# Kernel optimization log

Measured on AMD Instinct MI355X. Metric: run time of the kernel, lower is better.

## Reference

```python
import jax, jax.numpy as jnp
import numpy as np

B, S, N = 1, 128, 256
C_IN, C_H, C_OUT = 256, 32, 128
EPS = 1e-5


def setup_inputs() -> dict:
    key = jax.random.key(0)
    k_m, k_wa, k_wb, k_wo = jax.random.split(key, 4)
    m = jax.random.normal(k_m, (B, S, N, C_IN), dtype=jnp.float32)
    mask = jnp.ones((B, S, N), dtype=jnp.float32)
    gamma = jnp.ones((C_IN,), dtype=jnp.float32)
    beta = jnp.zeros((C_IN,), dtype=jnp.float32)
    # nn.Linear weights are (out, in)
    Wa = jax.random.normal(k_wa, (C_H, C_IN), dtype=jnp.float32) / np.sqrt(C_IN).astype(np.float32)
    Wb = jax.random.normal(k_wb, (C_H, C_IN), dtype=jnp.float32) / np.sqrt(C_IN).astype(np.float32)
    # proj_o is final_init (zeros) in the source; use small random weights so the
    # baseline output is non-trivial for correctness checking.
    Wo = jax.random.normal(k_wo, (C_OUT, C_H * C_H), dtype=jnp.float32) / np.sqrt(C_H * C_H).astype(np.float32)
    bo = jnp.zeros((C_OUT,), dtype=jnp.float32)
    return {"m": m, "mask": mask, "gamma": gamma, "beta": beta,
            "Wa": Wa, "Wb": Wb, "Wo": Wo, "bo": bo}


def reference(m, mask, gamma, beta, Wa, Wb, Wo, bo):
    # LayerNorm over c_in
    mu = jnp.mean(m, axis=-1, keepdims=True)
    var = jnp.mean((m - mu) ** 2, axis=-1, keepdims=True)
    mn = (m - mu) * jax.lax.rsqrt(var + EPS) * gamma + beta  # (B,S,N,c_in)

    mk = mask[..., None]  # (B,S,N,1)
    a = jnp.einsum('bsni,hi->bsnh', mn, Wa) * mk  # (B,S,N,c_h)
    b = jnp.einsum('bsni,hi->bsnh', mn, Wb) * mk  # (B,S,N,c_h)

    # pairwise mask count over S, clamped to >= 1
    num_mask = jnp.clip(jnp.einsum('bsi,bsj->bij', mask, mask), 1.0, None)  # (B,N,N)

    # outer-product mean over the sequence dim
    z = jnp.einsum('bsic,bsjd->bijcd', a, b)  # (B,N,N,c_h,c_h)
    z = z.reshape(z.shape[0], z.shape[1], z.shape[2], C_H * C_H)
    z = z / num_mask[..., None]

    return jnp.einsum('bijk,ok->bijo', z, Wo) + bo  # (B,N,N,c_out)
```

## Files before the change

### kernel.cpp

```cpp
#include <hip/hip_runtime.h>
#include <hip/hip_bf16.h>

#define S_DIM 128
#define N_DIM 256
#define CIN   256
#define CH    32
#define COUT  128

typedef __attribute__((ext_vector_type(8))) short bf16x8;
typedef __attribute__((ext_vector_type(4))) float f32x4;

__device__ __forceinline__ unsigned short f2bf(float f) {
  union { float f; unsigned int u; } v; v.f = f;
  unsigned int u = v.u;
  return (unsigned short)((u + 0x7FFFu + ((u >> 16) & 1u)) >> 16);
}

__device__ __forceinline__ unsigned int pk2(float x, float y) {
  float2 f2; f2.x = x; f2.y = y;
  __hip_bfloat162 h = __float22bfloat162_rn(f2);
  union { __hip_bfloat162 h; unsigned int u; } c; c.h = h;
  return c.u;
}

__global__ __launch_bounds__(256) void lnp_prep_kernel(
    const float* __restrict__ m, const float* __restrict__ mask,
    const float* __restrict__ gamma, const float* __restrict__ beta,
    const float* __restrict__ Wa, const float* __restrict__ Wb,
    const float* __restrict__ Wo,
    float* __restrict__ rnm, unsigned short* __restrict__ wo2,
    unsigned short* __restrict__ a_t, unsigned short* __restrict__ b_t) {
  const int b = blockIdx.x, t = threadIdx.x;
  if (b < 1024) {
    __shared__ __align__(16) unsigned short mn[32][264];
    __shared__ __align__(16) unsigned short wabs[64 * 256];
    const int i = b & 255, s0 = (b >> 8) * 32;
    const int w = t >> 6, l = t & 63, lq = l >> 4, lr = l & 15;

    #pragma unroll
    for (int it = 0; it < 8; it++) {
      const int gi = it * 256 + t;
      const int r = gi >> 5, g = gi & 31;
      const float* src = (r < 32) ? (Wa + r * 256 + g * 8)
                                  : (Wb + (r - 32) * 256 + g * 8);
      const int gp = (g & 16) | ((g ^ (r & 15)) & 15);
      unsigned short* dst = &wabs[r * 256 + gp * 8];
      const float4 v0 = *(const float4*)(src);
      const float4 v1 = *(const float4*)(src + 4);
      dst[0] = f2bf(v0.x); dst[1] = f2bf(v0.y); dst[2] = f2bf(v0.z); dst[3] = f2bf(v0.w);
      dst[4] = f2bf(v1.x); dst[5] = f2bf(v1.y); dst[6] = f2bf(v1.z); dst[7] = f2bf(v1.w);
    }

    const float4 g4 = *(const float4*)(gamma + l * 4);
    const float4 b4 = *(const float4*)(beta + l * 4);

    for (int rr = 0; rr < 8; rr++) {
      const int r = w * 8 + rr;
      const int s = s0 + r;
      const float4 v = *(const float4*)(m + ((size_t)(s * N_DIM + i)) * CIN + l * 4);
      float sum = v.x + v.y + v.z + v.w;
      float sq  = v.x * v.x + v.y * v.y + v.z * v.z + v.w * v.w;
      #pragma unroll
      for (int off = 32; off > 0; off >>= 1) {
        sum += __shfl_down(sum, off);
        sq  += __shfl_down(sq, off);
      }
      sum = __shfl(sum, 0); sq = __shfl(sq, 0);
      const float mu = sum * (1.0f / CIN);
      const float var = fmaxf(sq * (1.0f / CIN) - mu * mu, 0.0f);
      const float rs = rsqrtf(var + 1e-5f);
      const float mk = mask[s * N_DIM + i];
      ushort4 p;
      p.x = f2bf(((v.x - mu) * rs * g4.x + b4.x) * mk);
      p.y = f2bf(((v.y - mu) * rs * g4.y + b4.y) * mk);
      p.z = f2bf(((v.z - mu) * rs * g4.z + b4.z) * mk);
      p.w = f2bf(((v.w - mu) * rs * g4.w + b4.w) * mk);
      *(ushort4*)(&mn[r][l * 4]) = p;
    }
    __syncthreads();

    const int wm = w & 1;
    const int n2 = w >> 1;
    f32x4 acc0 = {0.f, 0.f, 0.f, 0.f}, acc1 = {0.f, 0.f, 0.f, 0.f};
    #pragma unroll
    for (int ks = 0; ks < 8; ks++) {
      const int k0 = ks * 32 + lq * 8;
      const int g = ks * 4 + lq;
      const int gp = (g & 16) | ((g ^ lr) & 15);
      const bf16x8 af = *(const bf16x8*)(&mn[wm * 16 + lr][k0]);
      const bf16x8 bf0 = *(const bf16x8*)(&wabs[(n2 * 32 + lr) * 256 + gp * 8]);
      const bf16x8 bf1 = *(const bf16x8*)(&wabs[(n2 * 32 + 16 + lr) * 256 + gp * 8]);
      acc0 = __builtin_amdgcn_mfma_f32_16x16x32_bf16(af, bf0, acc0, 0, 0, 0);
      acc1 = __builtin_amdgcn_mfma_f32_16x16x32_bf16(af, bf1, acc1, 0, 0, 0);
    }

    unsigned short* dst = (n2 == 0) ? a_t : b_t;
    const int scol = s0 + wm * 16 + lq * 4;
    ushort4 q0, q1;
    q0.x = f2bf(acc0[0]); q0.y = f2bf(acc0[1]); q0.z = f2bf(acc0[2]); q0.w = f2bf(acc0[3]);
    q1.x = f2bf(acc1[0]); q1.y = f2bf(acc1[1]); q1.z = f2bf(acc1[2]); q1.w = f2bf(acc1[3]);
    *(ushort4*)(dst + ((size_t)(i * CH + lr)) * S_DIM + scol) = q0;
    *(ushort4*)(dst + ((size_t)(i * CH + 16 + lr)) * S_DIM + scol) = q1;
  } else if (b < 1152) {
    const int r = b - 1024;
    #pragma unroll
    for (int q = 0; q < 4; q++) {
      const int f = r * 1024 + q * 256 + t;
      const int e = f & 7, l = (f >> 3) & 63, kk = (f >> 9) & 31, ot = f >> 14;
      const int kp = kk * 32 + (l >> 4) * 8 + e;
      const int c = kp & 31, d = kp >> 5;
      const int o = ot * 16 + (l & 15);
      wo2[f] = f2bf(Wo[o * 1024 + c * 32 + d]);
    }
  } else {
    const int i = b - 1152;
    float acc = 0.f;
    #pragma unroll 8
    for (int s = 0; s < S_DIM; s++)
      acc += mask[s * N_DIM + i] * mask[s * N_DIM + t];
    acc = fmaxf(acc, 1.0f);
    rnm[i * N_DIM + t] = 1.0f / acc;
  }
}

__global__ __launch_bounds__(1024, 4) void fused_kernel(
    const unsigned short* __restrict__ a_t, const unsigned short* __restrict__ b_t,
    const unsigned short* __restrict__ wo2, const float* __restrict__ rnm,
    const float* __restrict__ bo, float* __restrict__ out) {
  extern __shared__ __align__(16) unsigned short smem[];
  unsigned short* sA = smem;
  unsigned short* sB = smem + 32768;
  unsigned short* sZ = smem;

  const int t = threadIdx.x, w = t >> 6, l = t & 63;
  const int lq = l >> 4, lr = l & 15;
  const int bx = blockIdx.x, by = blockIdx.y;

  const unsigned short* srcA = a_t + (size_t)bx * 32768;
  const unsigned short* srcB = b_t + (size_t)by * 32768;
  #pragma unroll
  for (int it = 0; it < 4; it++) {
    const int idx = it * 1024 + t;
    const int r = idx >> 4, g = idx & 15;
    const int dst = r * 128 + ((g ^ (r & 15)) * 8);
    *(bf16x8*)(&sA[dst]) = *(const bf16x8*)(srcA + idx * 8);
    *(bf16x8*)(&sB[dst]) = *(const bf16x8*)(srcB + idx * 8);
  }
  __syncthreads();

  const int wy = (w >> 2) * 64, wx = (w & 3) * 64;
  f32x4 acc[4][4];
  #pragma unroll
  for (int a = 0; a < 4; a++)
    #pragma unroll
    for (int c = 0; c < 4; c++) acc[a][c] = (f32x4){0.f, 0.f, 0.f, 0.f};

  #pragma unroll
  for (int ks = 0; ks < 4; ks++) {
    const int g0 = ks * 4 + lq;
    bf16x8 afr[4], bfr[4];
    #pragma unroll
    for (int a = 0; a < 4; a++) {
      const int ra = wy + a * 16 + lr;
      afr[a] = *(const bf16x8*)(&sA[ra * 128 + ((g0 ^ (ra & 15)) * 8)]);
      const int rb = wx + a * 16 + lr;
      bfr[a] = *(const bf16x8*)(&sB[rb * 128 + ((g0 ^ (rb & 15)) * 8)]);
    }
    #pragma unroll
    for (int a = 0; a < 4; a++)
      #pragma unroll
      for (int c = 0; c < 4; c++)
        acc[a][c] = __builtin_amdgcn_mfma_f32_16x16x32_bf16(afr[a], bfr[c], acc[a][c], 0, 0, 0);
  }
  __syncthreads();

  #pragma unroll
  for (int a = 0; a < 4; a++) {
    #pragma unroll
    for (int c = 0; c < 4; c++) {
      const int zrb = wy + a * 16 + lq * 4;
      const int zc  = wx + c * 16 + lr;
      const int pair = (zrb >> 5) * 8 + (zc >> 5);
      const int off = (zc & 31) * 32 + (zrb & 31);
      const int g = off >> 3;
      const int gp = (g & ~7) | ((g ^ (g >> 3) ^ pair) & 7);
      uint2 q;
      q.x = pk2(acc[a][c][0], acc[a][c][1]);
      q.y = pk2(acc[a][c][2], acc[a][c][3]);
      *(uint2*)(&sZ[pair * 1024 + gp * 8 + (off & 7)]) = q;
    }
  }
  __syncthreads();

  const int pg = w & 3, og = w >> 2;
  const int p = pg * 16 + lr;
  const unsigned short* wbase0 = wo2 + (size_t)(og * 2) * 16384 + (size_t)l * 8;
  const unsigned short* wbase1 = wbase0 + 16384;
  f32x4 oa[2][2];
  oa[0][0] = oa[0][1] = oa[1][0] = oa[1][1] = (f32x4){0.f, 0.f, 0.f, 0.f};
  #pragma unroll 4
  for (int kk = 0; kk < 32; kk++) {
    const int g = kk * 4 + lq;
    const int gp = (g & ~7) | ((g ^ (g >> 3) ^ p) & 7);
    const bf16x8 zf = *(const bf16x8*)(&sZ[p * 1024 + gp * 8]);
    const bf16x8 w0 = *(const bf16x8*)(wbase0 + kk * 512);
    const bf16x8 w1 = *(const bf16x8*)(wbase1 + kk * 512);
    oa[0][kk & 1] = __builtin_amdgcn_mfma_f32_16x16x32_bf16(zf, w0, oa[0][kk & 1], 0, 0, 0);
    oa[1][kk & 1] = __builtin_amdgcn_mfma_f32_16x16x32_bf16(zf, w1, oa[1][kk & 1], 0, 0, 0);
  }

  #pragma unroll
  for (int f = 0; f < 2; f++) {
    const int o = (og * 2 + f) * 16 + lr;
    const float bov = bo[o];
    #pragma unroll
    for (int r = 0; r < 4; r++) {
      const int pair = pg * 16 + lq * 4 + r;
      const int ii = bx * 8 + (pair >> 3);
      const int jj = by * 8 + (pair & 7);
      const float sc = rnm[ii * N_DIM + jj];
      out[((size_t)(ii * N_DIM + jj)) * COUT + o] =
          (oa[f][0][r] + oa[f][1][r]) * sc + bov;
    }
  }
}

extern "C" void kernel_launch(void* const* d_in, const int* in_sizes, int n_in,
                              void* d_out, int out_size, void* d_ws, size_t ws_size,
                              hipStream_t stream) {
  const float* m     = (const float*)d_in[0];
  const float* mask  = (const float*)d_in[1];
  const float* gamma = (const float*)d_in[2];
  const float* beta  = (const float*)d_in[3];
  const float* Wa    = (const float*)d_in[4];
  const float* Wb    = (const float*)d_in[5];
  const float* Wo    = (const float*)d_in[6];
  const float* bo    = (const float*)d_in[7];
  float* out = (float*)d_out;

  char* ws = (char*)d_ws;
  float*          rnm = (float*)(ws);
  unsigned short* wo2 = (unsigned short*)(ws + 262144);
  unsigned short* a_t = (unsigned short*)(ws + 524288);
  unsigned short* b_t = (unsigned short*)(ws + 2621440);

  hipFuncSetAttribute((const void*)fused_kernel,
                      hipFuncAttributeMaxDynamicSharedMemorySize, 131072);

  lnp_prep_kernel<<<1408, 256, 0, stream>>>(m, mask, gamma, beta, Wa, Wb, Wo,
                                            rnm, wo2, a_t, b_t);
  fused_kernel<<<dim3(32, 32), 1024, 131072, stream>>>(a_t, b_t, wo2, rnm, bo, out);
}
```

Baseline: 157.2 us.

## Use 32x32x16 MFMA for output projection with split-K reduction via LDS

Rewrites the second GEMM (z times Wo) in the fused kernel to use 32x32x16 bf16 MFMA tiles instead of 16x16x32. Each wave now owns a 32-pair by 32-output tile and half the K range, and the two K halves are summed through an LDS scratch after an extra barrier. Wo is repacked in the prep kernel to match the new fragment layout. The aim is fewer MFMA issues and fewer global weight loads per output; the cost is an extra sync, LDS traffic for the partial sums, and half the waves sitting idle during the store phase.

```diff
diff --git a/kernel.cpp b/kernel.cpp
--- a/kernel.cpp
+++ b/kernel.cpp
@@ -9,6 +9,7 @@
 
 typedef __attribute__((ext_vector_type(8))) short bf16x8;
 typedef __attribute__((ext_vector_type(4))) float f32x4;
+typedef __attribute__((ext_vector_type(16))) float f32x16;
 
 __device__ __forceinline__ unsigned short f2bf(float f) {
   union { float f; unsigned int u; } v; v.f = f;
@@ -28,7 +29,7 @@
     const float* __restrict__ gamma, const float* __restrict__ beta,
     const float* __restrict__ Wa, const float* __restrict__ Wb,
     const float* __restrict__ Wo,
-    float* __restrict__ rnm, unsigned short* __restrict__ wo2,
+    float* __restrict__ rnm, unsigned short* __restrict__ wo3,
     unsigned short* __restrict__ a_t, unsigned short* __restrict__ b_t) {
   const int b = blockIdx.x, t = threadIdx.x;
   if (b < 1024) {
@@ -106,11 +107,12 @@
     #pragma unroll
     for (int q = 0; q < 4; q++) {
       const int f = r * 1024 + q * 256 + t;
-      const int e = f & 7, l = (f >> 3) & 63, kk = (f >> 9) & 31, ot = f >> 14;
-      const int kp = kk * 32 + (l >> 4) * 8 + e;
+      const int e = f & 7, l = (f >> 3) & 63;
+      const int step = (f >> 9) & 63, og = f >> 15;
+      const int kp = step * 16 + (l >> 5) * 8 + e;
       const int c = kp & 31, d = kp >> 5;
-      const int o = ot * 16 + (l & 15);
-      wo2[f] = f2bf(Wo[o * 1024 + c * 32 + d]);
+      const int o = og * 32 + (l & 31);
+      wo3[f] = f2bf(Wo[o * 1024 + c * 32 + d]);
     }
   } else {
     const int i = b - 1152;
@@ -125,7 +127,7 @@
 
 __global__ __launch_bounds__(1024, 4) void fused_kernel(
     const unsigned short* __restrict__ a_t, const unsigned short* __restrict__ b_t,
-    const unsigned short* __restrict__ wo2, const float* __restrict__ rnm,
+    const unsigned short* __restrict__ wo3, const float* __restrict__ rnm,
     const float* __restrict__ bo, float* __restrict__ out) {
   extern __shared__ __align__(16) unsigned short smem[];
   unsigned short* sA = smem;
@@ -192,35 +194,47 @@
   }
   __syncthreads();
 
-  const int pg = w & 3, og = w >> 2;
-  const int p = pg * 16 + lr;
-  const unsigned short* wbase0 = wo2 + (size_t)(og * 2) * 16384 + (size_t)l * 8;
-  const unsigned short* wbase1 = wbase0 + 16384;
-  f32x4 oa[2][2];
-  oa[0][0] = oa[0][1] = oa[1][0] = oa[1][1] = (f32x4){0.f, 0.f, 0.f, 0.f};
-  #pragma unroll 4
-  for (int kk = 0; kk < 32; kk++) {
-    const int g = kk * 4 + lq;
-    const int gp = (g & ~7) | ((g ^ (g >> 3) ^ p) & 7);
-    const bf16x8 zf = *(const bf16x8*)(&sZ[p * 1024 + gp * 8]);
-    const bf16x8 w0 = *(const bf16x8*)(wbase0 + kk * 512);
-    const bf16x8 w1 = *(const bf16x8*)(wbase1 + kk * 512);
-    oa[0][kk & 1] = __builtin_amdgcn_mfma_f32_16x16x32_bf16(zf, w0, oa[0][kk & 1], 0, 0, 0);
-    oa[1][kk & 1] = __builtin_amdgcn_mfma_f32_16x16x32_bf16(zf, w1, oa[1][kk & 1], 0, 0, 0);
-  }
-
-  #pragma unroll
-  for (int f = 0; f < 2; f++) {
-    const int o = (og * 2 + f) * 16 + lr;
+  const int ph = w & 1, og = (w >> 1) & 3, kh = w >> 3;
+  const int pair2 = ph * 32 + (l & 31);
+  const int zbase = pair2 * 1024;
+  const unsigned short* wop =
+      wo3 + ((size_t)(og * 64 + kh * 32) * 64 + l) * 8;
+  f32x16 acc2;
+  #pragma unroll
+  for (int r = 0; r < 16; r++) acc2[r] = 0.f;
+
+  #pragma unroll 8
+  for (int j = 0; j < 32; j++) {
+    const int s = kh * 32 + j;
+    const int g = s * 2 + (l >> 5);
+    const int gp = (g & ~7) | ((g ^ (g >> 3) ^ pair2) & 7);
+    const bf16x8 zf = *(const bf16x8*)(&sZ[zbase + gp * 8]);
+    const bf16x8 wf = *(const bf16x8*)(wop + j * 512);
+    acc2 = __builtin_amdgcn_mfma_f32_32x32x16_bf16(zf, wf, acc2, 0, 0, 0);
+  }
+  __syncthreads();
+
+  float* fpart = (float*)sZ;
+  const int job = w & 7;
+  if (kh) {
+    #pragma unroll
+    for (int r = 0; r < 16; r++)
+      fpart[(job * 16 + r) * 64 + l] = acc2[r];
+  }
+  __syncthreads();
+
+  if (!kh) {
+    const int o = og * 32 + (l & 31);
     const float bov = bo[o];
     #pragma unroll
-    for (int r = 0; r < 4; r++) {
-      const int pair = pg * 16 + lq * 4 + r;
-      const int ii = bx * 8 + (pair >> 3);
-      const int jj = by * 8 + (pair & 7);
+    for (int r = 0; r < 16; r++) {
+      const int row = (r & 3) + 8 * (r >> 2) + 4 * (l >> 5);
+      const int pr = ph * 32 + row;
+      const int ii = bx * 8 + (pr >> 3);
+      const int jj = by * 8 + (pr & 7);
       const float sc = rnm[ii * N_DIM + jj];
       out[((size_t)(ii * N_DIM + jj)) * COUT + o] =
-          (oa[f][0][r] + oa[f][1][r]) * sc + bov;
+          (acc2[r] + fpart[(job * 16 + r) * 64 + l]) * sc + bov;
     }
   }
 }
@@ -240,7 +254,7 @@
 
   char* ws = (char*)d_ws;
   float*          rnm = (float*)(ws);
-  unsigned short* wo2 = (unsigned short*)(ws + 262144);
+  unsigned short* wo3 = (unsigned short*)(ws + 262144);
   unsigned short* a_t = (unsigned short*)(ws + 524288);
   unsigned short* b_t = (unsigned short*)(ws + 2621440);
 
@@ -248,6 +262,6 @@
                       hipFuncAttributeMaxDynamicSharedMemorySize, 131072);
 
   lnp_prep_kernel<<<1408, 256, 0, stream>>>(m, mask, gamma, beta, Wa, Wb, Wo,
-                                            rnm, wo2, a_t, b_t);
-  fused_kernel<<<dim3(32, 32), 1024, 131072, stream>>>(a_t, b_t, wo2, rnm, bo, out);
-}
+                                            rnm, wo3, a_t, b_t);
+  fused_kernel<<<dim3(32, 32), 1024, 131072, stream>>>(a_t, b_t, wo3, rnm, bo, out);
+}
```

Result: faster. 146.6 us (-6.8%).
